# Kernel optimization log

Measured on AMD Instinct MI355X. Metric: run time of the kernel, lower is better.

## Reference

```python
import jax, jax.numpy as jnp
import numpy as np

EPS = 1e-6
SINKHORN_ITERS = 8
TEMPERATURE = 1.0
B, N, D = 4, 8192, 512
E, OUT = 8, 512
H = 1


def setup_inputs() -> dict:
    key = jax.random.key(0)
    k1, k2, k3 = jax.random.split(key, 3)
    x = jax.random.normal(k1, (B, N, D), dtype=jnp.float32)
    gate_weight = jax.random.normal(k2, (H, D, E), dtype=jnp.float32)
    experts = jax.random.normal(k3, (E, D, OUT), dtype=jnp.float32) * 0.02
    return {"x": x, "gate_weight": gate_weight, "experts": experts}


def _sinkhorn(logits):
    # logits: (b, h, n, e). log(clamp(.,eps)) then alternating row/col log-normalization.
    t = jnp.log(jnp.clip(logits, EPS)) / TEMPERATURE
    for _ in range(SINKHORN_ITERS):
        t = t - jax.nn.logsumexp(t, axis=-2, keepdims=True)  # normalize over tokens n
        t = t - jax.nn.logsumexp(t, axis=-1, keepdims=True)  # normalize over experts e
    return jnp.exp(t)


def reference(x, gate_weight, experts):
    b, n, d = x.shape
    e = experts.shape[0]
    m = n // e  # tokens per expert
    xh = x[:, None, :, :]  # b 1 n d  (single-headed -> h=1)
    gate_logits = jnp.einsum('bhnd,hde->bhne', xh, gate_weight)
    gates = _sinkhorn(gate_logits)  # b h n e
    # topk over token dim n, per expert: move n to last axis for lax.top_k
    g_t = jnp.swapaxes(gates, -1, -2)  # b h e n
    vals, idx = jax.lax.top_k(g_t, m)  # (b h e m), (b h e m)
    gate_values = jnp.transpose(vals, (2, 0, 1, 3))[..., None]  # e b h m 1
    # gather routed tokens: routed[e,b,h,m,d] = x[b,h,idx[b,h,e,m],d]
    routed = jnp.take_along_axis(xh[:, :, None, :, :], idx[..., None], axis=3)  # b h e m d
    routed = jnp.transpose(routed, (2, 0, 1, 3, 4))  # e b h m d
    expert_w = experts[:, None, :, :]  # e h i o with h=1 (rearrange 'e i o -> e 1 i o')
    outputs = jnp.einsum('ebhmi,ehio->ebhmo', routed, expert_w)  # e b h m o
    outputs = outputs * gate_values
    # scatter back (set semantics, matching einx set_at)
    bh_idx = idx.reshape(b, 1, e * m)  # b h (e m)
    bh_vals = jnp.transpose(outputs, (1, 2, 0, 3, 4)).reshape(b, 1, e * m, outputs.shape[-1])
    def scat(i1, v1):
        return jnp.zeros((n, v1.shape[-1]), dtype=v1.dtype).at[i1].set(v1)
    routed_back = jax.vmap(jax.vmap(scat))(bh_idx, bh_vals)  # b h n o
    return routed_back[:, 0]  # b n o
```

## Files before the change

### kernel.cpp

```cpp
#include <hip/hip_runtime.h>
#include <hip/hip_bf16.h>

#define BB 4
#define NN 8192
#define DD 512
#define EE 8
#define OUTD 512
#define TOPM 1024
#define EPSV 1e-6f
#define ITERS 8

using s16x8 = __attribute__((ext_vector_type(8))) short;
using f32x4 = __attribute__((ext_vector_type(4))) float;
typedef unsigned long long u64;

__device__ __forceinline__ unsigned short f2bf(float f) {
  unsigned u = __float_as_uint(f);
  return (unsigned short)((u + 0x7FFFu + ((u >> 16) & 1u)) >> 16);
}

__device__ __forceinline__ void gll16(const void* g, void* l) {
  __builtin_amdgcn_global_load_lds((const __attribute__((address_space(1))) void*)g,
                                   (__attribute__((address_space(3))) void*)l, 16, 0, 0);
}

__global__ __launch_bounds__(256) void k_gate(const float* __restrict__ x,
                                              const float* __restrict__ gw,
                                              float* __restrict__ t0,
                                              unsigned short* __restrict__ xbf,
                                              int* __restrict__ eo,
                                              int* __restrict__ counts,
                                              const float* __restrict__ W,
                                              unsigned short* __restrict__ WT) {
  const int tid = threadIdx.x;
  if (blockIdx.x >= 2048) {
    __shared__ float tl[32][33];
    const int widx = blockIdx.x - 2048;
    const int e = widx >> 8, rem = widx & 255;
    const int k0 = (rem >> 4) * 32, n0 = (rem & 15) * 32;
    const int ty = tid >> 5, tx = tid & 31;
    const float* src = W + ((long)e * DD + k0) * OUTD + n0;
#pragma unroll
    for (int j = 0; j < 4; ++j)
      tl[ty + j * 8][tx] = src[(long)(ty + j * 8) * OUTD + tx];
    __syncthreads();
    unsigned short* dst = WT + ((long)e * OUTD + n0) * DD + k0;
#pragma unroll
    for (int j = 0; j < 4; ++j)
      dst[(long)(ty + j * 8) * DD + tx] = f2bf(tl[tx][ty + j * 8]);
    return;
  }
  if (tid < 16) eo[blockIdx.x * 16 + tid] = -1;
  if (blockIdx.x == 0 && tid >= 64 && tid < 64 + BB * EE) counts[tid - 64] = 0;
  const int lane = tid & 63;
  const int w    = tid >> 6;
  float gwf[64];
  const float* gb = gw + (lane * 8) * EE;
#pragma unroll
  for (int q = 0; q < 16; ++q) {
    float4 t = *(const float4*)(gb + q * 4);
    gwf[q * 4 + 0] = t.x; gwf[q * 4 + 1] = t.y;
    gwf[q * 4 + 2] = t.z; gwf[q * 4 + 3] = t.w;
  }
#pragma unroll
  for (int q = 0; q < 64; ++q) asm volatile("" : "+v"(gwf[q]));

  const long row0 = (long)blockIdx.x * 16 + w * 4;
  float4 xa[4], xb[4];
#pragma unroll
  for (int i = 0; i < 4; ++i) {
    const float* xr = x + (row0 + i) * DD + lane * 8;
    xa[i] = *(const float4*)(xr);
    xb[i] = *(const float4*)(xr + 4);
  }
  float vout[4];
#pragma unroll
  for (int i = 0; i < 4; ++i) {
    float xv[8] = {xa[i].x, xa[i].y, xa[i].z, xa[i].w,
                   xb[i].x, xb[i].y, xb[i].z, xb[i].w};
    s16x8 xo;
#pragma unroll
    for (int j = 0; j < 8; ++j) xo[j] = (short)f2bf(xv[j]);
    *(s16x8*)(xbf + (row0 + i) * DD + lane * 8) = xo;

    float acc[8] = {0.f,0.f,0.f,0.f,0.f,0.f,0.f,0.f};
#pragma unroll
    for (int q = 0; q < 8; ++q)
#pragma unroll
      for (int e = 0; e < 8; ++e) acc[e] += xv[q] * gwf[q * 8 + e];
    const bool o1 = lane & 1;
    float own, oth, b0, b1, b2, b3, c0, c1, v;
    own = o1 ? acc[1] : acc[0]; oth = o1 ? acc[0] : acc[1];
    b0 = own + __shfl_xor(oth, 1);
    own = o1 ? acc[3] : acc[2]; oth = o1 ? acc[2] : acc[3];
    b1 = own + __shfl_xor(oth, 1);
    own = o1 ? acc[5] : acc[4]; oth = o1 ? acc[4] : acc[5];
    b2 = own + __shfl_xor(oth, 1);
    own = o1 ? acc[7] : acc[6]; oth = o1 ? acc[6] : acc[7];
    b3 = own + __shfl_xor(oth, 1);
    const bool o2 = lane & 2;
    own = o2 ? b1 : b0; oth = o2 ? b0 : b1;
    c0 = own + __shfl_xor(oth, 2);
    own = o2 ? b3 : b2; oth = o2 ? b2 : b3;
    c1 = own + __shfl_xor(oth, 2);
    const bool o4 = lane & 4;
    own = o4 ? c1 : c0; oth = o4 ? c0 : c1;
    v = own + __shfl_xor(oth, 4);
    v += __shfl_xor(v, 8);
    v += __shfl_xor(v, 16);
    v += __shfl_xor(v, 32);
    vout[i] = v;
  }
  const int gsel = lane >> 3;
  float vsel = vout[0];
  vsel = (gsel == 1) ? vout[1] : vsel;
  vsel = (gsel == 2) ? vout[2] : vsel;
  vsel = (gsel == 3) ? vout[3] : vsel;
  if (lane < 32) t0[row0 * EE + lane] = logf(fmaxf(vsel, EPSV));
}

__global__ __attribute__((amdgpu_waves_per_eu(4, 4)))
__launch_bounds__(1024) void k_topk(const float* __restrict__ t0,
                                    float* __restrict__ R,
                                    float* __restrict__ C,
                                    int* __restrict__ expert_of) {
  __shared__ unsigned key[NN];
  __shared__ int hist[4096];
  __shared__ int bcast[2];
  __shared__ int wsum[16];
  __shared__ float ws[16][8], Csh[8], Ssh[8];
  const int b = blockIdx.x >> 3, e = blockIdx.x & 7;
  const int tid = threadIdx.x;
  const int wv = tid >> 6, ln = tid & 63;
  const float* tb = t0 + (long)b * NN * EE;

  float E[8][8], u[8], dl[8];
#pragma unroll
  for (int j = 0; j < 8; ++j) {
    const float* p = tb + (long)(j * 1024 + tid) * EE;
    float4 a = *(const float4*)p, b4 = *(const float4*)(p + 4);
    E[j][0] = expf(a.x);  E[j][1] = expf(a.y);
    E[j][2] = expf(a.z);  E[j][3] = expf(a.w);
    E[j][4] = expf(b4.x); E[j][5] = expf(b4.y);
    E[j][6] = expf(b4.z); E[j][7] = expf(b4.w);
    key[j * 1024 + tid] = __float_as_uint(p[e]);
    u[j] = 1.f;
  }
#pragma unroll
  for (int j = 0; j < 8; ++j)
#pragma unroll
    for (int e2 = 0; e2 < 8; ++e2)
      asm volatile("" : "+v"(E[j][e2]));
  for (int it = 0; it < ITERS; ++it) {
    float P[8] = {0.f,0.f,0.f,0.f,0.f,0.f,0.f,0.f};
#pragma unroll
    for (int j = 0; j < 8; ++j)
#pragma unroll
      for (int e2 = 0; e2 < 8; ++e2) P[e2] += E[j][e2] * u[j];
#pragma unroll
    for (int d = 1; d <= 4; d <<= 1) {
#pragma unroll
      for (int e2 = 0; e2 < 8; ++e2) {
        float tmp = __shfl_xor(P[e2], d);
        P[e2] += ((ln & d) == (e2 & d)) ? tmp : 0.f;
      }
    }
    float pv = P[0];
#pragma unroll
    for (int e2 = 1; e2 < 8; ++e2) pv = ((ln & 7) == e2) ? P[e2] : pv;
#pragma unroll
    for (int d = 8; d < 64; d <<= 1) pv += __shfl_xor(pv, d);
    if (ln < 8) ws[wv][ln] = pv;
    __syncthreads();
    if (tid < 64) {
      const int q = ln >> 3, e2 = ln & 7;
      float s = ws[q][e2] + ws[q + 8][e2];
#pragma unroll
      for (int d = 8; d < 64; d <<= 1) s += __shfl_xor(s, d);
      if (ln < 8) { Csh[ln] = 1.f / s; Ssh[ln] = s; }
    }
    __syncthreads();
    float vv[8];
#pragma unroll
    for (int e2 = 0; e2 < 8; ++e2) vv[e2] = Csh[e2];
#pragma unroll
    for (int j = 0; j < 8; ++j) {
      float d0 = E[j][0] * vv[0];
#pragma unroll
      for (int e2 = 1; e2 < 8; ++e2) d0 += E[j][e2] * vv[e2];
      dl[j] = d0;
      u[j] = 1.f / d0;
    }
    __syncthreads();
  }
  if (e == 0) {
#pragma unroll
    for (int j = 0; j < 8; ++j) R[(long)b * NN + j * 1024 + tid] = logf(dl[j]);
    if (tid < 8) C[b * EE + tid] = logf(Ssh[tid]);
  }

  {
    int4 z4 = make_int4(0, 0, 0, 0);
    *(int4*)&hist[tid * 4] = z4;
  }
  __syncthreads();
#pragma unroll
  for (int j = 0; j < 8; ++j) {
    const int n = j * 1024 + tid;
    float f = __uint_as_float(key[n]) - logf(dl[j]);
    unsigned uk = __float_as_uint(f);
    uk = (uk & 0x80000000u) ? ~uk : (uk | 0x80000000u);
    key[n] = uk;
    atomicAdd(&hist[uk >> 20], 1);
  }
  __syncthreads();

  unsigned prefix = 0;
  int k = TOPM;
  for (int pass = 0; pass < 3; ++pass) {
    const int4 h4 = *(const int4*)&hist[tid * 4];
    const int s3 = h4.w, s2 = h4.z + s3, s1 = h4.y + s2, s0 = h4.x + s1;
    int inc = s0;
#pragma unroll
    for (int d = 1; d < 64; d <<= 1) {
      int o = __shfl_down(inc, d);
      if (ln + d < 64) inc += o;
    }
    if (ln == 0) wsum[wv] = inc;
    __syncthreads();
    if (tid == 0) {
      int run = 0;
      for (int w2 = 15; w2 >= 0; --w2) { int t2 = wsum[w2]; wsum[w2] = run; run += t2; }
    }
    __syncthreads();
    const int above = wsum[wv] + (inc - s0);
    const int c0 = above + s0, c1 = above + s1, c2 = above + s2, c3 = above + s3;
    if (c0 >= k && c1 < k)    { bcast[0] = k - c1;    bcast[1] = tid * 4 + 0; }
    if (c1 >= k && c2 < k)    { bcast[0] = k - c2;    bcast[1] = tid * 4 + 1; }
    if (c2 >= k && c3 < k)    { bcast[0] = k - c3;    bcast[1] = tid * 4 + 2; }
    if (c3 >= k && above < k) { bcast[0] = k - above; bcast[1] = tid * 4 + 3; }
    __syncthreads();
    k = bcast[0];
    const unsigned bin = (unsigned)bcast[1];
    if (pass == 0)      prefix = bin << 20;
    else if (pass == 1) prefix |= bin << 8;
    else                prefix |= bin;
    if (pass == 2) break;
    {
      int4 z4 = make_int4(0, 0, 0, 0);
      *(int4*)&hist[tid * 4] = z4;
    }
    __syncthreads();
    if (pass == 0) {
      const unsigned pa = prefix >> 20;
      for (int n = tid; n < NN; n += 1024) {
        unsigned uk = key[n];
        if ((uk >> 20) == pa) atomicAdd(&hist[(uk >> 8) & 4095], 1);
      }
    } else {
      const unsigned pb = prefix >> 8;
      for (int n = tid; n < NN; n += 1024) {
        unsigned uk = key[n];
        if ((uk >> 8) == pb) atomicAdd(&hist[uk & 255], 1);
      }
    }
    __syncthreads();
  }
  const unsigned theta = prefix;
  const int need = k;
  const int base = tid * 8;
  int c = 0;
#pragma unroll
  for (int j = 0; j < 8; ++j) if (key[base + j] == theta) ++c;
  int inc2 = c;
#pragma unroll
  for (int d = 1; d < 64; d <<= 1) {
    int o = __shfl_up(inc2, d);
    if (ln >= d) inc2 += o;
  }
  if (ln == 63) wsum[wv] = inc2;
  __syncthreads();
  if (tid == 0) {
    int runv = 0;
    for (int i = 0; i < 16; ++i) { int t2 = wsum[i]; wsum[i] = runv; runv += t2; }
  }
  __syncthreads();
  int run = wsum[wv] + inc2 - c;
  int* eo = expert_of + b * NN;
  for (int j = 0; j < 8; ++j) {
    int n = base + j;
    unsigned uk = key[n];
    bool sel = false;
    if (uk > theta) sel = true;
    else if (uk == theta) { if (run < need) sel = true; ++run; }
    if (sel) atomicMax(&eo[n], e);
  }
}

__global__ __launch_bounds__(256) void k_post(const int* __restrict__ expert_of,
                                              const float* __restrict__ t0,
                                              const float* __restrict__ R,
                                              const float* __restrict__ C,
                                              int* __restrict__ counts,
                                              int* __restrict__ lists,
                                              float* __restrict__ gvals) {
  __shared__ int hist8[8], base8[8];
  const int tid = threadIdx.x;
  if (tid < 8) hist8[tid] = 0;
  __syncthreads();
  const long i = (long)blockIdx.x * 256 + tid;
  const int b = (int)(i >> 13);
  const int e = expert_of[i];
  int lpos = -1;
  if (e >= 0) lpos = atomicAdd(&hist8[e], 1);
  __syncthreads();
  if (tid < 8 && hist8[tid] > 0)
    base8[tid] = atomicAdd(&counts[b * EE + tid], hist8[tid]);
  __syncthreads();
  if (e >= 0) {
    const int n = (int)(i & (NN - 1));
    const int be = b * EE + e;
    const int slot = be * TOPM + base8[e] + lpos;
    lists[slot] = n;
    gvals[slot] = expf(t0[i * EE + e] - C[be] - R[i]);
  }
}

__global__ __launch_bounds__(256) void k_gemm(const unsigned short* __restrict__ xbf,
                                              const unsigned short* __restrict__ WT,
                                              const int* __restrict__ counts,
                                              const int* __restrict__ lists,
                                              const float* __restrict__ gvals,
                                              const int* __restrict__ eo,
                                              float* __restrict__ out) {
  const int tid = threadIdx.x;
  if (blockIdx.x >= 1024) {
    const int row = (blockIdx.x - 1024) * 4 + (tid >> 6);
    if (eo[row] >= 0) return;
    const int ln = tid & 63;
    float4 z = make_float4(0.f, 0.f, 0.f, 0.f);
    float4* p = (float4*)(out + (long)row * OUTD) + ln;
    p[0] = z; p[64] = z;
    return;
  }
  const int id = blockIdx.x;
  const int xq = id >> 8;
  const int be = (id >> 3) & 31;
  const int yq = id & 7;
  const int b = be >> 3, e = be & 7;
  const int cnt = counts[be];
  const int r0 = yq * 128;
  if (r0 >= cnt) return;
  const int c0 = xq * 128;

  __shared__ unsigned short As[128 * 64];
  __shared__ unsigned short Bs[128 * 64];
  __shared__ int   rowTok[128];
  __shared__ float rowG[128];

  if (tid < 128) {
    int r = r0 + tid;
    rowTok[tid] = (r < cnt) ? lists[be * TOPM + r] : -1;
    rowG[tid]   = (r < cnt) ? gvals[be * TOPM + r] : 0.f;
  }
  __syncthreads();

  const int w = tid >> 6, l = tid & 63;
  const int rbase = w * 32 + (l >> 3);
  const int sL = l & 7;
  const unsigned short* xb_b = xbf + (long)b * NN * DD;
  const unsigned short* wt_e = WT + (long)e * OUTD * DD;
  int tokc[4]; int sGa[4];
#pragma unroll
  for (int c = 0; c < 4; ++c) {
    int r = rbase + c * 8;
    int tk = rowTok[r]; if (tk < 0) tk = 0;
    tokc[c] = tk;
    sGa[c] = (sL ^ (r & 7)) * 8;
  }

  const int wr = w >> 1, wc = w & 1;
  const int fr = l & 15, fq = l >> 4;
  int aoff[4][2], boff[4][2];
#pragma unroll
  for (int m = 0; m < 4; ++m) {
#pragma unroll
    for (int kk = 0; kk < 2; ++kk) {
      int row = wr * 64 + m * 16 + fr;
      aoff[m][kk] = row * 64 + (((fq + 4 * kk) ^ (row & 7)) * 8);
      int col = wc * 64 + m * 16 + fr;
      boff[m][kk] = col * 64 + (((fq + 4 * kk) ^ (col & 7)) * 8);
    }
  }

  f32x4 acc[4][4] = {};

#define STAGE(kb) {                                                          \
    int ko = (kb) * 64;                                                      \
    _Pragma("unroll")                                                        \
    for (int c = 0; c < 4; ++c) {                                            \
      int r = rbase + c * 8;                                                 \
      gll16(xb_b + (long)tokc[c] * DD + ko + sGa[c],                         \
            As + (w * 32 + c * 8) * 64);                                     \
      gll16(wt_e + (long)(c0 + r) * DD + ko + sGa[c],                        \
            Bs + (w * 32 + c * 8) * 64);                                     \
    }                                                                        \
  }

  STAGE(0);
  for (int kb = 0; kb < 8; ++kb) {
    __syncthreads();
    s16x8 af[4][2], bf_[4][2];
#pragma unroll
    for (int m = 0; m < 4; ++m) {
      af[m][0] = *(const s16x8*)(As + aoff[m][0]);
      af[m][1] = *(const s16x8*)(As + aoff[m][1]);
      bf_[m][0] = *(const s16x8*)(Bs + boff[m][0]);
      bf_[m][1] = *(const s16x8*)(Bs + boff[m][1]);
    }
    __syncthreads();
    if (kb < 7) STAGE(kb + 1);
#pragma unroll
    for (int kk = 0; kk < 2; ++kk)
#pragma unroll
      for (int m = 0; m < 4; ++m)
#pragma unroll
        for (int n = 0; n < 4; ++n)
          acc[m][n] = __builtin_amdgcn_mfma_f32_16x16x32_bf16(af[m][kk], bf_[n][kk], acc[m][n], 0, 0, 0);
  }
#undef STAGE

#pragma unroll
  for (int m = 0; m < 4; ++m) {
    int rbase2 = wr * 64 + m * 16 + fq * 4;
    int tok[4]; float g[4];
#pragma unroll
    for (int j = 0; j < 4; ++j) { tok[j] = rowTok[rbase2 + j]; g[j] = rowG[rbase2 + j]; }
#pragma unroll
    for (int n = 0; n < 4; ++n) {
      int col = c0 + wc * 64 + n * 16 + fr;
#pragma unroll
      for (int j = 0; j < 4; ++j) {
        if (tok[j] >= 0)
          out[((long)b * NN + tok[j]) * OUTD + col] = acc[m][n][j] * g[j];
      }
    }
  }
}

extern "C" void kernel_launch(void* const* d_in, const int* in_sizes, int n_in,
                              void* d_out, int out_size, void* d_ws, size_t ws_size,
                              hipStream_t stream) {
  const float* x  = (const float*)d_in[0];
  const float* gw = (const float*)d_in[1];
  const float* ex = (const float*)d_in[2];
  float* out = (float*)d_out;

  char* wsb = (char*)d_ws;
  float*          t0     = (float*)(wsb);
  unsigned short* xbf    = (unsigned short*)(wsb + (1l << 20));
  unsigned short* WT     = (unsigned short*)(wsb + (33l << 20));
  const long base = 37l << 20;
  float*          R      = (float*)(wsb + base);
  int*            eo     = (int*)  (wsb + base + (128l << 10));
  int*            lists  = (int*)  (wsb + base + (256l << 10));
  float*          gvals  = (float*)(wsb + base + (384l << 10));
  float*          C      = (float*)(wsb + base + (512l << 10));
  int*            counts = (int*)  (wsb + base + (512l << 10) + 1024);

  k_gate<<<2048 + 2048, 256, 0, stream>>>(x, gw, t0, xbf, eo, counts, ex, WT);
  k_topk<<<BB * EE, 1024, 0, stream>>>(t0, R, C, eo);
  k_post<<<128, 256, 0, stream>>>(eo, t0, R, C, counts, lists, gvals);
  k_gemm<<<1024 + (BB * NN) / 4, 256, 0, stream>>>(xbf, WT, counts, lists, gvals, eo, out);
}
```

Baseline: 101.3 us.

## Split gate GEMV K-dimension across waves and reduce partials in shared memory

Changes the gate-logit part of the prep kernel: each wave now owns a quarter of the D dimension for all 16 rows of the block, instead of full rows for 4 rows. Each lane holds only 16 gate weights instead of 64, and partial sums are combined across waves through shared memory behind a barrier. The aim is lower register pressure and better occupancy while streaming x. The cost is four times as many shuffle reductions per wave, narrower per-lane loads, and an extra block-wide sync.

```diff
diff --git a/kernel.cpp b/kernel.cpp
--- a/kernel.cpp
+++ b/kernel.cpp
@@ -50,44 +50,34 @@
       dst[(long)(ty + j * 8) * DD + tx] = f2bf(tl[tx][ty + j * 8]);
     return;
   }
+  __shared__ float ws[16][4][8];
   if (tid < 16) eo[blockIdx.x * 16 + tid] = -1;
   if (blockIdx.x == 0 && tid >= 64 && tid < 64 + BB * EE) counts[tid - 64] = 0;
   const int lane = tid & 63;
-  const int w    = tid >> 6;
-  float gwf[64];
-  const float* gb = gw + (lane * 8) * EE;
-#pragma unroll
-  for (int q = 0; q < 16; ++q) {
-    float4 t = *(const float4*)(gb + q * 4);
-    gwf[q * 4 + 0] = t.x; gwf[q * 4 + 1] = t.y;
-    gwf[q * 4 + 2] = t.z; gwf[q * 4 + 3] = t.w;
-  }
-#pragma unroll
-  for (int q = 0; q < 64; ++q) asm volatile("" : "+v"(gwf[q]));
-
-  const long row0 = (long)blockIdx.x * 16 + w * 4;
-  float4 xa[4], xb[4];
-#pragma unroll
-  for (int i = 0; i < 4; ++i) {
-    const float* xr = x + (row0 + i) * DD + lane * 8;
-    xa[i] = *(const float4*)(xr);
-    xb[i] = *(const float4*)(xr + 4);
-  }
-  float vout[4];
-#pragma unroll
-  for (int i = 0; i < 4; ++i) {
-    float xv[8] = {xa[i].x, xa[i].y, xa[i].z, xa[i].w,
-                   xb[i].x, xb[i].y, xb[i].z, xb[i].w};
-    s16x8 xo;
-#pragma unroll
-    for (int j = 0; j < 8; ++j) xo[j] = (short)f2bf(xv[j]);
-    *(s16x8*)(xbf + (row0 + i) * DD + lane * 8) = xo;
-
-    float acc[8] = {0.f,0.f,0.f,0.f,0.f,0.f,0.f,0.f};
-#pragma unroll
-    for (int q = 0; q < 8; ++q)
-#pragma unroll
-      for (int e = 0; e < 8; ++e) acc[e] += xv[q] * gwf[q * 8 + e];
+  const int wq   = tid >> 6;
+  const int k2   = wq * 128 + lane * 2;
+  const float* gp = gw + (long)k2 * EE;
+  const float4 g0 = *(const float4*)(gp);
+  const float4 g1 = *(const float4*)(gp + 4);
+  const float4 g2 = *(const float4*)(gp + 8);
+  const float4 g3 = *(const float4*)(gp + 12);
+
+  const long row0 = (long)blockIdx.x * 16;
+  for (int i = 0; i < 16; ++i) {
+    const long row = row0 + i;
+    const float2 xv = *(const float2*)(x + row * DD + k2);
+    *(unsigned*)(xbf + row * DD + k2) =
+        ((unsigned)f2bf(xv.y) << 16) | (unsigned)f2bf(xv.x);
+
+    float acc[8];
+    acc[0] = xv.x * g0.x + xv.y * g2.x;
+    acc[1] = xv.x * g0.y + xv.y * g2.y;
+    acc[2] = xv.x * g0.z + xv.y * g2.z;
+    acc[3] = xv.x * g0.w + xv.y * g2.w;
+    acc[4] = xv.x * g1.x + xv.y * g3.x;
+    acc[5] = xv.x * g1.y + xv.y * g3.y;
+    acc[6] = xv.x * g1.z + xv.y * g3.z;
+    acc[7] = xv.x * g1.w + xv.y * g3.w;
     const bool o1 = lane & 1;
     float own, oth, b0, b1, b2, b3, c0, c1, v;
     own = o1 ? acc[1] : acc[0]; oth = o1 ? acc[0] : acc[1];
@@ -109,14 +99,14 @@
     v += __shfl_xor(v, 8);
     v += __shfl_xor(v, 16);
     v += __shfl_xor(v, 32);
-    vout[i] = v;
-  }
-  const int gsel = lane >> 3;
-  float vsel = vout[0];
-  vsel = (gsel == 1) ? vout[1] : vsel;
-  vsel = (gsel == 2) ? vout[2] : vsel;
-  vsel = (gsel == 3) ? vout[3] : vsel;
-  if (lane < 32) t0[row0 * EE + lane] = logf(fmaxf(vsel, EPSV));
+    if (lane < 8) ws[i][wq][lane] = v;
+  }
+  __syncthreads();
+  if (tid < 128) {
+    const int row = tid >> 3, e = tid & 7;
+    float s = ws[row][0][e] + ws[row][1][e] + ws[row][2][e] + ws[row][3][e];
+    t0[row0 * EE + tid] = logf(fmaxf(s, EPSV));
+  }
 }
 
 __global__ __attribute__((amdgpu_waves_per_eu(4, 4)))
```

Result: no change. 101.2 us, median of 2 (-0.1%).
